# Kernel tuning notes

Hardware: AMD Instinct MI355X
Metric: run time of the kernel (lower is better)

The kernel has to match this reference:

```python
import jax, jax.numpy as jnp
import numpy as np

# Hard-coded dims from the module: 76 subcarriers * 12 data OFDM symbols = 912 data REs,
# QPSK (2 bits/sym), rate 1/2 -> n=1824, k=912; 4 tx streams, 8 rx antennas.
B, S, K = 512, 4, 912      # batch, streams, info bits (= data REs per stream)
R = 8                       # rx antennas
D = K                       # data resource elements per stream
N_CODE = 2 * K              # coded bits
SH1, SH2 = 7, 150           # circulant shifts of the LDPC-like code
BP_ITERS = 10
INV_SQRT2 = 0.7071067811865476

# check c connects info vars {c, c-7, c-150 (mod K)} and parity var K+c -> check degree 4
_c = np.arange(K)
VAR_IDX = jnp.asarray(np.stack([_c % K, (_c - SH1) % K, (_c - SH2) % K, K + _c], axis=1), jnp.int32)  # [K,4]


def setup_inputs() -> dict:
    key = jax.random.key(0)
    k1, k2, k3, k4, k5 = jax.random.split(key, 5)
    return {
        "b_bits": jax.random.randint(k1, (B, S, K), 0, 2, dtype=jnp.int32),
        "h_real": jax.random.normal(k2, (B, D, R, S), dtype=jnp.float32),
        "h_imag": jax.random.normal(k3, (B, D, R, S), dtype=jnp.float32),
        "n_real": jax.random.normal(k4, (B, D, R), dtype=jnp.float32),
        "n_imag": jax.random.normal(k5, (B, D, R), dtype=jnp.float32),
        "ebno_db": 10,
    }


def _bp_decode(llr):
    """Min-sum BP decode. llr: [B,S,N_CODE] demapper LLRs (log p1/p0). Returns hard info bits."""
    L = (-llr).reshape(B * S, N_CODE)          # internal convention log(p0/p1)
    vflat = VAR_IDX.reshape(-1)
    c2v = jnp.zeros((B * S, K, 4), L.dtype)
    pos = jnp.arange(4)
    for _ in range(BP_ITERS):
        ext = jnp.zeros_like(L).at[:, vflat].add(c2v.reshape(B * S, -1))
        tot = L + ext
        m_vc = tot[:, VAR_IDX] - c2v           # [BS,K,4] var->check
        a = jnp.abs(m_vc)
        srt = jnp.sort(a, -1)
        min1, min2 = srt[..., 0:1], srt[..., 1:2]
        amin = jnp.argmin(a, -1, keepdims=True)
        excl = jnp.where(pos == amin, min2, min1)   # leave-one-out min
        s = jnp.where(m_vc < 0, -1.0, 1.0)
        s_excl = jnp.prod(s, -1, keepdims=True) * s  # sign product excluding self
        c2v = s_excl * excl
    ext = jnp.zeros_like(L).at[:, vflat].add(c2v.reshape(B * S, -1))
    tot = L + ext
    return (tot[:, :K] < 0).astype(jnp.int32).reshape(B, S, K)


def reference(b_bits, h_real, h_imag, n_real, n_imag, ebno_db):
    no = 10.0 ** (-float(ebno_db) / 10.0)  # ebnodb2no with 2 bits/sym * rate 1/2
    # --- LDPC-like systematic circulant encode: p = A b mod 2, c = [b | p] ---
    p = (b_bits + jnp.roll(b_bits, SH1, -1) + jnp.roll(b_bits, SH2, -1)) % 2
    c = jnp.concatenate([b_bits, p], -1)                    # [B,S,N_CODE]
    # --- Gray QPSK mapper ---
    cb = c.reshape(B, S, K, 2).astype(jnp.float32)
    x = ((1.0 - 2.0 * cb[..., 0]) + 1j * (1.0 - 2.0 * cb[..., 1])) * INV_SQRT2  # [B,S,D]
    x_rg = jnp.transpose(x, (0, 2, 1))                      # [B,D,S]
    # --- normalized Rayleigh MIMO channel per RE + AWGN ---
    h = ((h_real + 1j * h_imag) * INV_SQRT2).astype(jnp.complex64)  # [B,D,R,S], E|h|^2=1
    noise = (n_real + 1j * n_imag).astype(jnp.complex64) * np.float32(np.sqrt(no * 0.5))
    y = jnp.einsum('bdrs,bds->bdr', h, x_rg) + noise        # [B,D,R]
    # --- per-RE LMMSE equalizer with Sionna-style bias normalization ---
    hH = jnp.conj(jnp.swapaxes(h, -1, -2))                  # [B,D,S,R]
    A = jnp.einsum('bdsr,bdrt->bdst', hH, h) + jnp.asarray(no, h.dtype) * jnp.eye(S, dtype=h.dtype)
    G = jnp.linalg.solve(A, hH)                             # [B,D,S,R]
    z = jnp.einsum('bdsr,bdr->bds', G, y)
    dgg = jnp.clip(jnp.real(jnp.einsum('bdsr,bdrs->bds', G, h)), 1e-6, 1.0 - 1e-6)
    x_hat = z / dgg.astype(jnp.complex64)
    no_eff = (1.0 - dgg) / dgg                              # [B,D,S]
    # --- exact APP QPSK demapper: llr = log p1/p0 ---
    scale = -2.0 * np.float32(np.sqrt(2.0)) / no_eff
    llr = jnp.stack([scale * jnp.real(x_hat), scale * jnp.imag(x_hat)], -1)  # [B,D,S,2]
    llr = jnp.transpose(llr, (0, 2, 1, 3)).reshape(B, S, N_CODE)
    # --- BP decode ---
    b_hat = _bp_decode(llr)
    return b_bits, b_hat
```

## Files before the change

### kernel.cpp

```cpp
#include <hip/hip_runtime.h>

#define B_ 512
#define S_ 4
#define K_ 912
#define R_ 8
#define D_ 912
#define NCODE 1824
#define BSK (B_*S_*K_)
#define BP_ITERS 10
#define NTH 228
#define CODES_OFF 16

__global__ void setup_kernel(const int* __restrict__ ebno, float* __restrict__ cst) {
  int ei = ebno[0];
  float ef = (ei >= -100 && ei <= 100) ? (float)ei : __int_as_float(ei);
  double no_d = pow(10.0, -(double)ef / 10.0);
  cst[0] = (float)no_d;
  cst[1] = (float)sqrt(no_d * 0.5);
}

__global__ __launch_bounds__(256) void pack_codes_kernel(
    const int* __restrict__ bbits, unsigned char* __restrict__ codes) {
  int g = blockIdx.x * 256 + threadIdx.x;
  int b = g / D_;
  int d = g - b * D_;
  int k2 = 2 * d;
  unsigned code = 0;
#pragma unroll
  for (int s = 0; s < S_; ++s) {
    const int* bb = bbits + (b * S_ + s) * K_;
    unsigned c0, c1;
    if (k2 < K_) {
      c0 = (unsigned)bb[k2];
      c1 = (unsigned)bb[k2 + 1];
    } else {
      int j0 = k2 - K_, j1 = k2 + 1 - K_;
      int j0a = j0 - 7;   if (j0a < 0) j0a += K_;
      int j0b = j0 - 150; if (j0b < 0) j0b += K_;
      c0 = (unsigned)(bb[j0] + bb[j0a] + bb[j0b]) & 1u;
      int j1a = j1 - 7;   if (j1a < 0) j1a += K_;
      int j1b = j1 - 150; if (j1b < 0) j1b += K_;
      c1 = (unsigned)(bb[j1] + bb[j1a] + bb[j1b]) & 1u;
    }
    code |= (c0 << (2 * s)) | (c1 << (2 * s + 1));
  }
  codes[g] = (unsigned char)code;
}

#define BFLY1(v) { v += __shfl_xor(v, 1); }

__global__ __launch_bounds__(256) void mmse_llr_kernel(
    const float* __restrict__ hre, const float* __restrict__ him,
    const float* __restrict__ nre, const float* __restrict__ nim,
    const float* __restrict__ cst, const unsigned char* __restrict__ codes,
    float* __restrict__ outf) {
#pragma clang fp contract(off)
  __shared__ float4 sre[1024];
  __shared__ float4 sim[1024];
  int tid = threadIdx.x;
  int t = blockIdx.x * 256 + tid;
  int g = t >> 1;
  int half = t & 1;
  int b = g / D_;
  int d = g - b * D_;
  int k2 = 2 * d;

  const float no_f = cst[0];
  const float nscale = cst[1];
  const float INV2 = 0.70710678118654752440f;

  const float4* hre4 = reinterpret_cast<const float4*>(hre);
  const float4* him4 = reinterpret_cast<const float4*>(him);
  size_t base = (size_t)blockIdx.x * 1024;
#pragma unroll
  for (int j = 0; j < 4; ++j) {
    int m = j * 256 + tid;
    int slot = (m & ~3) | ((m & 3) ^ ((m >> 3) & 3));
    sre[slot] = hre4[base + m];
    sim[slot] = him4[base + m];
  }

  float4 nr4v = reinterpret_cast<const float4*>(nre)[t];
  float4 ni4v = reinterpret_cast<const float4*>(nim)[t];
  unsigned code = codes[g];
  __syncthreads();

  float xr[S_], xq[S_];
#pragma unroll
  for (int s = 0; s < S_; ++s) {
    unsigned c0 = (code >> (2 * s)) & 1u;
    unsigned c1 = (code >> (2 * s + 1)) & 1u;
    xr[s] = __uint_as_float(0x3F3504F3u ^ (c0 << 31));
    xq[s] = __uint_as_float(0x3F3504F3u ^ (c1 << 31));
  }

  int gl = tid >> 1;
  int vb = gl * 8 + half * 4;
  int key = gl & 3;
  float4 hRq[4], hIq[4];
#pragma unroll
  for (int q = 0; q < 4; ++q) {
    int slot = vb + (q ^ key);
    hRq[q ^ key ? 0 : 0] = hRq[0];
  }
#pragma unroll
  for (int q = 0; q < 4; ++q) {
    hRq[q] = sre[vb + (q ^ key)];
    hIq[q] = sim[vb + (q ^ key)];
  }

  float nrv[4] = {nr4v.x, nr4v.y, nr4v.z, nr4v.w};
  float niv[4] = {ni4v.x, ni4v.y, ni4v.z, ni4v.w};

  float Ad0=0.f, Ad1=0.f, Ad2=0.f, Ad3=0.f;
  float A10r=0.f,A10i=0.f,A20r=0.f,A20i=0.f,A21r=0.f,A21i=0.f;
  float A30r=0.f,A30i=0.f,A31r=0.f,A31i=0.f,A32r=0.f,A32i=0.f;
  float w0r=0.f,w0i=0.f,w1r=0.f,w1i=0.f,w2r=0.f,w2i=0.f,w3r=0.f,w3i=0.f;

#pragma unroll
  for (int q = 0; q < 4; ++q) {
    float4 h4r = hRq[q];
    float4 h4i = hIq[q];
    float hr0=h4r.x*INV2, hr1=h4r.y*INV2, hr2=h4r.z*INV2, hr3=h4r.w*INV2;
    float hi0=h4i.x*INV2, hi1=h4i.y*INV2, hi2=h4i.z*INV2, hi3=h4i.w*INV2;
    float yr = 0.f, yi = 0.f;
    yr += hr0*xr[0] - hi0*xq[0]; yi += hr0*xq[0] + hi0*xr[0];
    yr += hr1*xr[1] - hi1*xq[1]; yi += hr1*xq[1] + hi1*xr[1];
    yr += hr2*xr[2] - hi2*xq[2]; yi += hr2*xq[2] + hi2*xr[2];
    yr += hr3*xr[3] - hi3*xq[3]; yi += hr3*xq[3] + hi3*xr[3];
    yr += nrv[q]*nscale; yi += niv[q]*nscale;
    Ad0 += hr0*hr0 + hi0*hi0;
    Ad1 += hr1*hr1 + hi1*hi1;
    Ad2 += hr2*hr2 + hi2*hi2;
    Ad3 += hr3*hr3 + hi3*hi3;
    A10r += hr1*hr0 + hi1*hi0;  A10i += hr1*hi0 - hi1*hr0;
    A20r += hr2*hr0 + hi2*hi0;  A20i += hr2*hi0 - hi2*hr0;
    A21r += hr2*hr1 + hi2*hi1;  A21i += hr2*hi1 - hi2*hr1;
    A30r += hr3*hr0 + hi3*hi0;  A30i += hr3*hi0 - hi3*hr0;
    A31r += hr3*hr1 + hi3*hi1;  A31i += hr3*hi1 - hi3*hr1;
    A32r += hr3*hr2 + hi3*hi2;  A32i += hr3*hi2 - hi3*hr2;
    w0r += hr0*yr + hi0*yi;  w0i += hr0*yi - hi0*yr;
    w1r += hr1*yr + hi1*yi;  w1i += hr1*yi - hi1*yr;
    w2r += hr2*yr + hi2*yi;  w2i += hr2*yi - hi2*yr;
    w3r += hr3*yr + hi3*yi;  w3i += hr3*yi - hi3*yr;
  }

  BFLY1(Ad0) BFLY1(Ad1) BFLY1(Ad2) BFLY1(Ad3)
  BFLY1(A10r) BFLY1(A10i) BFLY1(A20r) BFLY1(A20i) BFLY1(A21r) BFLY1(A21i)
  BFLY1(A30r) BFLY1(A30i) BFLY1(A31r) BFLY1(A31i) BFLY1(A32r) BFLY1(A32i)
  BFLY1(w0r) BFLY1(w0i) BFLY1(w1r) BFLY1(w1i)
  BFLY1(w2r) BFLY1(w2i) BFLY1(w3r) BFLY1(w3i)

  float Dv0 = Ad0 + no_f;
  float iD0 = 1.0f / Dv0;
  float L10r = A10r*iD0, L10i = A10i*iD0;
  float L20r = A20r*iD0, L20i = A20i*iD0;
  float L30r = A30r*iD0, L30i = A30i*iD0;
  float Dv1 = Ad1 + no_f - (L10r*L10r + L10i*L10i)*Dv0;
  float iD1 = 1.0f / Dv1;
  float t21r = A21r - (L20r*L10r + L20i*L10i)*Dv0;
  float t21i = A21i - (L20i*L10r - L20r*L10i)*Dv0;
  float L21r = t21r*iD1, L21i = t21i*iD1;
  float t31r = A31r - (L30r*L10r + L30i*L10i)*Dv0;
  float t31i = A31i - (L30i*L10r - L30r*L10i)*Dv0;
  float L31r = t31r*iD1, L31i = t31i*iD1;
  float Dv2 = Ad2 + no_f - (L20r*L20r + L20i*L20i)*Dv0 - (L21r*L21r + L21i*L21i)*Dv1;
  float iD2 = 1.0f / Dv2;
  float t32r = A32r - (L30r*L20r + L30i*L20i)*Dv0 - (L31r*L21r + L31i*L21i)*Dv1;
  float t32i = A32i - (L30i*L20r - L30r*L20i)*Dv0 - (L31i*L21r - L31r*L21i)*Dv1;
  float L32r = t32r*iD2, L32i = t32i*iD2;
  float Dv3 = Ad3 + no_f - (L30r*L30r + L30i*L30i)*Dv0 - (L31r*L31r + L31i*L31i)*Dv1
                        - (L32r*L32r + L32i*L32i)*Dv2;
  float iD3 = 1.0f / Dv3;

  float c0r = w0r, c0i = w0i;
  float c1r = w1r - (L10r*c0r - L10i*c0i);
  float c1i = w1i - (L10r*c0i + L10i*c0r);
  float c2r = w2r - (L20r*c0r - L20i*c0i) - (L21r*c1r - L21i*c1i);
  float c2i = w2i - (L20r*c0i + L20i*c0r) - (L21r*c1i + L21i*c1r);
  float c3r = w3r - (L30r*c0r - L30i*c0i) - (L31r*c1r - L31i*c1i) - (L32r*c2r - L32i*c2i);
  float c3i = w3i - (L30r*c0i + L30i*c0r) - (L31r*c1i + L31i*c1r) - (L32r*c2i + L32i*c2r);
  c0r *= iD0; c0i *= iD0;
  c1r *= iD1; c1i *= iD1;
  c2r *= iD2; c2i *= iD2;
  c3r *= iD3; c3i *= iD3;
  float z3r = c3r, z3i = c3i;
  float z2r = c2r - (L32r*z3r + L32i*z3i);
  float z2i = c2i - (L32r*z3i - L32i*z3r);
  float z1r = c1r - (L21r*z2r + L21i*z2i) - (L31r*z3r + L31i*z3i);
  float z1i = c1i - (L21r*z2i - L21i*z2r) - (L31r*z3i - L31i*z3r);
  float z0r = c0r - (L10r*z1r + L10i*z1i) - (L20r*z2r + L20i*z2i) - (L30r*z3r + L30i*z3i);
  float z0i = c0i - (L10r*z1i - L10i*z1r) - (L20r*z2i - L20i*z2r) - (L30r*z3i - L30i*z3r);

  float M10r = -L10r, M10i = -L10i;
  float M21r = -L21r, M21i = -L21i;
  float M32r = -L32r, M32i = -L32i;
  float M20r = -L20r - (L21r*M10r - L21i*M10i);
  float M20i = -L20i - (L21r*M10i + L21i*M10r);
  float M31r = -L31r - (L32r*M21r - L32i*M21i);
  float M31i = -L31i - (L32r*M21i + L32i*M21r);
  float M30r = -L30r - (L31r*M10r - L31i*M10i) - (L32r*M20r - L32i*M20i);
  float M30i = -L30i - (L31r*M10i + L31i*M10r) - (L32r*M20i + L32i*M20r);
  float Ai0 = iD0 + (M10r*M10r + M10i*M10i)*iD1 + (M20r*M20r + M20i*M20i)*iD2
                  + (M30r*M30r + M30i*M30i)*iD3;
  float Ai1 = iD1 + (M21r*M21r + M21i*M21i)*iD2 + (M31r*M31r + M31i*M31i)*iD3;
  float Ai2 = iD2 + (M32r*M32r + M32i*M32i)*iD3;
  float Ai3 = iD3;

  float zrv[4] = {z0r, z1r, z2r, z3r};
  float ziv[4] = {z0i, z1i, z2i, z3i};
  float Aiv[4] = {Ai0, Ai1, Ai2, Ai3};

#pragma unroll
  for (int j = 0; j < 2; ++j) {
    int s = half * 2 + j;
    float dgg = 1.0f - no_f * Aiv[s];
    float dg = fminf(fmaxf(dgg, 1e-6f), (float)(1.0 - 1e-6));
    float xhr = zrv[s] / dg;
    float xhi = ziv[s] / dg;
    float noe = (1.0f - dg) / dg;
    float sc = -2.8284270763397217f / noe;
    float2 o;
    o.x = -(sc * xhr);
    o.y = -(sc * xhi);
    size_t w = (size_t)(b * S_ + s);
    if (k2 < K_) {
      *reinterpret_cast<float2*>(outf + w * K_ + k2) = o;
    } else {
      *reinterpret_cast<float2*>(outf + (size_t)BSK + w * K_ + (k2 - K_)) = o;
    }
  }
}

__global__ __launch_bounds__(256) void bp_kernel(const int* __restrict__ bbits,
                                                 int* __restrict__ out) {
#pragma clang fp contract(off)
  __shared__ float tot[K_];
  __shared__ float E0[K_];
  __shared__ float E1[K_];
  __shared__ float E2[K_];
  int w = blockIdx.x;
  int tid = threadIdx.x;
  const float* outf = (const float*)out;
  bool act = tid < NTH;

  float Lv[4], LP[4];
  float c0v[4] = {0.f,0.f,0.f,0.f};
  float c1v[4] = {0.f,0.f,0.f,0.f};
  float c2v_[4] = {0.f,0.f,0.f,0.f};
  float c3v[4] = {0.f,0.f,0.f,0.f};

  if (act) {
#pragma unroll
    for (int k = 0; k < 4; ++k) {
      int n = tid + NTH * k;
      Lv[k] = outf[(size_t)w * K_ + n];
      LP[k] = outf[(size_t)BSK + (size_t)w * K_ + n];
      E0[n] = 0.f; E1[n] = 0.f; E2[n] = 0.f;
    }
  }
  __syncthreads();

  for (int it = 0; it < BP_ITERS; ++it) {
    if (act) {
#pragma unroll
      for (int k = 0; k < 4; ++k) {
        int n = tid + NTH * k;
        tot[n] = Lv[k] + ((E0[n] + E1[n]) + E2[n]);
      }
    }
    __syncthreads();
    if (act) {
#pragma unroll
      for (int k = 0; k < 4; ++k) {
        int c = tid + NTH * k;
        int i1 = c - 7;   if (i1 < 0) i1 += K_;
        int i2 = c - 150; if (i2 < 0) i2 += K_;
        float m0 = tot[c]  - c0v[k];
        float m1 = tot[i1] - c1v[k];
        float m2 = tot[i2] - c2v_[k];
        float totP = LP[k] + c3v[k];
        float m3 = totP - c3v[k];
        float a0 = fabsf(m0), a1 = fabsf(m1), a2 = fabsf(m2), a3 = fabsf(m3);
        float t01 = fminf(a0, a1), t23 = fminf(a2, a3);
        float e0 = fminf(a1, t23);
        float e1 = fminf(a0, t23);
        float e2 = fminf(t01, a3);
        float e3 = fminf(t01, a2);
        unsigned s0 = __float_as_uint(m0) & 0x80000000u;
        unsigned s1 = __float_as_uint(m1) & 0x80000000u;
        unsigned s2 = __float_as_uint(m2) & 0x80000000u;
        unsigned s3 = __float_as_uint(m3) & 0x80000000u;
        unsigned sp = (s0 ^ s1) ^ (s2 ^ s3);
        float n0 = __uint_as_float(__float_as_uint(e0) ^ (sp ^ s0));
        float n1 = __uint_as_float(__float_as_uint(e1) ^ (sp ^ s1));
        float n2 = __uint_as_float(__float_as_uint(e2) ^ (sp ^ s2));
        float n3 = __uint_as_float(__float_as_uint(e3) ^ (sp ^ s3));
        c0v[k] = n0; c1v[k] = n1; c2v_[k] = n2; c3v[k] = n3;
        E0[c] = n0; E1[i1] = n1; E2[i2] = n2;
      }
    }
    __syncthreads();
  }

  if (act) {
#pragma unroll
    for (int k = 0; k < 4; ++k) {
      int n = tid + NTH * k;
      float ttt = Lv[k] + ((E0[n] + E1[n]) + E2[n]);
      out[(size_t)BSK + (size_t)w * K_ + n] = (ttt < 0.f) ? 1 : 0;
      out[(size_t)w * K_ + n] = bbits[(size_t)w * K_ + n];
    }
  }
}

extern "C" void kernel_launch(void* const* d_in, const int* in_sizes, int n_in,
                              void* d_out, int out_size, void* d_ws, size_t ws_size,
                              hipStream_t stream) {
  const int*   b_bits = (const int*)d_in[0];
  const float* h_real = (const float*)d_in[1];
  const float* h_imag = (const float*)d_in[2];
  const float* n_real = (const float*)d_in[3];
  const float* n_imag = (const float*)d_in[4];
  const int*   ebno   = (const int*)d_in[5];
  int* out = (int*)d_out;
  float* cst = (float*)d_ws;
  unsigned char* codes = (unsigned char*)d_ws + CODES_OFF;

  setup_kernel<<<1, 1, 0, stream>>>(ebno, cst);
  pack_codes_kernel<<<(B_ * D_) / 256, 256, 0, stream>>>(b_bits, codes);
  mmse_llr_kernel<<<(B_ * D_ * 2) / 256, 256, 0, stream>>>(
      h_real, h_imag, n_real, n_imag, cst, codes, (float*)d_out);
  bp_kernel<<<B_ * S_, 256, 0, stream>>>(b_bits, out);
}
```

Before: 65.55 us.

## Restructure MMSE kernel: one thread per RE, two REs per thread, staged loads

The MMSE/LLR kernel changes from two threads per resource element (with shuffle reductions) to one thread handling two whole resource elements. Each 128-thread block covers 256 REs and streams the channel through shared memory in four phases of two rx antennas each. This removes the cross-lane butterflies and duplicated Cholesky solve, raising work per thread. In exchange, the 24-float accumulators for two REs raise register pressure, the grid has fewer threads, and each phase adds a barrier.

Measured after the change: 98.76 us. 50.7% more time.

```diff
diff --git a/kernel.cpp b/kernel.cpp
--- a/kernel.cpp
+++ b/kernel.cpp
@@ -3,13 +3,13 @@
 #define B_ 512
 #define S_ 4
 #define K_ 912
-#define R_ 8
 #define D_ 912
-#define NCODE 1824
 #define BSK (B_*S_*K_)
 #define BP_ITERS 10
 #define NTH 228
 #define CODES_OFF 16
+#define THB 128
+#define GRPB 256
 
 __global__ void setup_kernel(const int* __restrict__ ebno, float* __restrict__ cst) {
   int ei = ebno[0];
@@ -47,173 +47,112 @@
   codes[g] = (unsigned char)code;
 }
 
-#define BFLY1(v) { v += __shfl_xor(v, 1); }
-
-__global__ __launch_bounds__(256) void mmse_llr_kernel(
-    const float* __restrict__ hre, const float* __restrict__ him,
-    const float* __restrict__ nre, const float* __restrict__ nim,
-    const float* __restrict__ cst, const unsigned char* __restrict__ codes,
-    float* __restrict__ outf) {
+struct AccT {
+  float Ad0, Ad1, Ad2, Ad3;
+  float A10r, A10i, A20r, A20i, A21r, A21i;
+  float A30r, A30i, A31r, A31i, A32r, A32i;
+  float w0r, w0i, w1r, w1i, w2r, w2i, w3r, w3i;
+};
+
+__device__ __forceinline__ void accum(AccT& A, float4 h4r, float4 h4i,
+                                      const float* xr, const float* xq,
+                                      float nr, float ni, float nscale) {
 #pragma clang fp contract(off)
-  __shared__ float4 sre[1024];
-  __shared__ float4 sim[1024];
-  int tid = threadIdx.x;
-  int t = blockIdx.x * 256 + tid;
-  int g = t >> 1;
-  int half = t & 1;
-  int b = g / D_;
-  int d = g - b * D_;
-  int k2 = 2 * d;
-
-  const float no_f = cst[0];
-  const float nscale = cst[1];
   const float INV2 = 0.70710678118654752440f;
-
-  const float4* hre4 = reinterpret_cast<const float4*>(hre);
-  const float4* him4 = reinterpret_cast<const float4*>(him);
-  size_t base = (size_t)blockIdx.x * 1024;
-#pragma unroll
-  for (int j = 0; j < 4; ++j) {
-    int m = j * 256 + tid;
-    int slot = (m & ~3) | ((m & 3) ^ ((m >> 3) & 3));
-    sre[slot] = hre4[base + m];
-    sim[slot] = him4[base + m];
-  }
-
-  float4 nr4v = reinterpret_cast<const float4*>(nre)[t];
-  float4 ni4v = reinterpret_cast<const float4*>(nim)[t];
-  unsigned code = codes[g];
-  __syncthreads();
-
-  float xr[S_], xq[S_];
-#pragma unroll
-  for (int s = 0; s < S_; ++s) {
-    unsigned c0 = (code >> (2 * s)) & 1u;
-    unsigned c1 = (code >> (2 * s + 1)) & 1u;
-    xr[s] = __uint_as_float(0x3F3504F3u ^ (c0 << 31));
-    xq[s] = __uint_as_float(0x3F3504F3u ^ (c1 << 31));
-  }
-
-  int gl = tid >> 1;
-  int vb = gl * 8 + half * 4;
-  int key = gl & 3;
-  float4 hRq[4], hIq[4];
-#pragma unroll
-  for (int q = 0; q < 4; ++q) {
-    int slot = vb + (q ^ key);
-    hRq[q ^ key ? 0 : 0] = hRq[0];
-  }
-#pragma unroll
-  for (int q = 0; q < 4; ++q) {
-    hRq[q] = sre[vb + (q ^ key)];
-    hIq[q] = sim[vb + (q ^ key)];
-  }
-
-  float nrv[4] = {nr4v.x, nr4v.y, nr4v.z, nr4v.w};
-  float niv[4] = {ni4v.x, ni4v.y, ni4v.z, ni4v.w};
-
-  float Ad0=0.f, Ad1=0.f, Ad2=0.f, Ad3=0.f;
-  float A10r=0.f,A10i=0.f,A20r=0.f,A20i=0.f,A21r=0.f,A21i=0.f;
-  float A30r=0.f,A30i=0.f,A31r=0.f,A31i=0.f,A32r=0.f,A32i=0.f;
-  float w0r=0.f,w0i=0.f,w1r=0.f,w1i=0.f,w2r=0.f,w2i=0.f,w3r=0.f,w3i=0.f;
-
-#pragma unroll
-  for (int q = 0; q < 4; ++q) {
-    float4 h4r = hRq[q];
-    float4 h4i = hIq[q];
-    float hr0=h4r.x*INV2, hr1=h4r.y*INV2, hr2=h4r.z*INV2, hr3=h4r.w*INV2;
-    float hi0=h4i.x*INV2, hi1=h4i.y*INV2, hi2=h4i.z*INV2, hi3=h4i.w*INV2;
-    float yr = 0.f, yi = 0.f;
-    yr += hr0*xr[0] - hi0*xq[0]; yi += hr0*xq[0] + hi0*xr[0];
-    yr += hr1*xr[1] - hi1*xq[1]; yi += hr1*xq[1] + hi1*xr[1];
-    yr += hr2*xr[2] - hi2*xq[2]; yi += hr2*xq[2] + hi2*xr[2];
-    yr += hr3*xr[3] - hi3*xq[3]; yi += hr3*xq[3] + hi3*xr[3];
-    yr += nrv[q]*nscale; yi += niv[q]*nscale;
-    Ad0 += hr0*hr0 + hi0*hi0;
-    Ad1 += hr1*hr1 + hi1*hi1;
-    Ad2 += hr2*hr2 + hi2*hi2;
-    Ad3 += hr3*hr3 + hi3*hi3;
-    A10r += hr1*hr0 + hi1*hi0;  A10i += hr1*hi0 - hi1*hr0;
-    A20r += hr2*hr0 + hi2*hi0;  A20i += hr2*hi0 - hi2*hr0;
-    A21r += hr2*hr1 + hi2*hi1;  A21i += hr2*hi1 - hi2*hr1;
-    A30r += hr3*hr0 + hi3*hi0;  A30i += hr3*hi0 - hi3*hr0;
-    A31r += hr3*hr1 + hi3*hi1;  A31i += hr3*hi1 - hi3*hr1;
-    A32r += hr3*hr2 + hi3*hi2;  A32i += hr3*hi2 - hi3*hr2;
-    w0r += hr0*yr + hi0*yi;  w0i += hr0*yi - hi0*yr;
-    w1r += hr1*yr + hi1*yi;  w1i += hr1*yi - hi1*yr;
-    w2r += hr2*yr + hi2*yi;  w2i += hr2*yi - hi2*yr;
-    w3r += hr3*yr + hi3*yi;  w3i += hr3*yi - hi3*yr;
-  }
-
-  BFLY1(Ad0) BFLY1(Ad1) BFLY1(Ad2) BFLY1(Ad3)
-  BFLY1(A10r) BFLY1(A10i) BFLY1(A20r) BFLY1(A20i) BFLY1(A21r) BFLY1(A21i)
-  BFLY1(A30r) BFLY1(A30i) BFLY1(A31r) BFLY1(A31i) BFLY1(A32r) BFLY1(A32i)
-  BFLY1(w0r) BFLY1(w0i) BFLY1(w1r) BFLY1(w1i)
-  BFLY1(w2r) BFLY1(w2i) BFLY1(w3r) BFLY1(w3i)
-
-  float Dv0 = Ad0 + no_f;
+  float hr0 = h4r.x * INV2, hr1 = h4r.y * INV2, hr2 = h4r.z * INV2, hr3 = h4r.w * INV2;
+  float hi0 = h4i.x * INV2, hi1 = h4i.y * INV2, hi2 = h4i.z * INV2, hi3 = h4i.w * INV2;
+  float yr = 0.f, yi = 0.f;
+  yr += hr0 * xr[0] - hi0 * xq[0]; yi += hr0 * xq[0] + hi0 * xr[0];
+  yr += hr1 * xr[1] - hi1 * xq[1]; yi += hr1 * xq[1] + hi1 * xr[1];
+  yr += hr2 * xr[2] - hi2 * xq[2]; yi += hr2 * xq[2] + hi2 * xr[2];
+  yr += hr3 * xr[3] - hi3 * xq[3]; yi += hr3 * xq[3] + hi3 * xr[3];
+  yr += nr * nscale; yi += ni * nscale;
+  A.Ad0 += hr0 * hr0 + hi0 * hi0;
+  A.Ad1 += hr1 * hr1 + hi1 * hi1;
+  A.Ad2 += hr2 * hr2 + hi2 * hi2;
+  A.Ad3 += hr3 * hr3 + hi3 * hi3;
+  A.A10r += hr1 * hr0 + hi1 * hi0;  A.A10i += hr1 * hi0 - hi1 * hr0;
+  A.A20r += hr2 * hr0 + hi2 * hi0;  A.A20i += hr2 * hi0 - hi2 * hr0;
+  A.A21r += hr2 * hr1 + hi2 * hi1;  A.A21i += hr2 * hi1 - hi2 * hr1;
+  A.A30r += hr3 * hr0 + hi3 * hi0;  A.A30i += hr3 * hi0 - hi3 * hr0;
+  A.A31r += hr3 * hr1 + hi3 * hi1;  A.A31i += hr3 * hi1 - hi3 * hr1;
+  A.A32r += hr3 * hr2 + hi3 * hi2;  A.A32i += hr3 * hi2 - hi3 * hr2;
+  A.w0r += hr0 * yr + hi0 * yi;  A.w0i += hr0 * yi - hi0 * yr;
+  A.w1r += hr1 * yr + hi1 * yi;  A.w1i += hr1 * yi - hi1 * yr;
+  A.w2r += hr2 * yr + hi2 * yi;  A.w2i += hr2 * yi - hi2 * yr;
+  A.w3r += hr3 * yr + hi3 * yi;  A.w3i += hr3 * yi - hi3 * yr;
+}
+
+__device__ __forceinline__ void solve_write(const AccT& a, float no_f, int g,
+                                            float* __restrict__ outf) {
+#pragma clang fp contract(off)
+  float Dv0 = a.Ad0 + no_f;
   float iD0 = 1.0f / Dv0;
-  float L10r = A10r*iD0, L10i = A10i*iD0;
-  float L20r = A20r*iD0, L20i = A20i*iD0;
-  float L30r = A30r*iD0, L30i = A30i*iD0;
-  float Dv1 = Ad1 + no_f - (L10r*L10r + L10i*L10i)*Dv0;
+  float L10r = a.A10r * iD0, L10i = a.A10i * iD0;
+  float L20r = a.A20r * iD0, L20i = a.A20i * iD0;
+  float L30r = a.A30r * iD0, L30i = a.A30i * iD0;
+  float Dv1 = a.Ad1 + no_f - (L10r * L10r + L10i * L10i) * Dv0;
   float iD1 = 1.0f / Dv1;
-  float t21r = A21r - (L20r*L10r + L20i*L10i)*Dv0;
-  float t21i = A21i - (L20i*L10r - L20r*L10i)*Dv0;
-  float L21r = t21r*iD1, L21i = t21i*iD1;
-  float t31r = A31r - (L30r*L10r + L30i*L10i)*Dv0;
-  float t31i = A31i - (L30i*L10r - L30r*L10i)*Dv0;
-  float L31r = t31r*iD1, L31i = t31i*iD1;
-  float Dv2 = Ad2 + no_f - (L20r*L20r + L20i*L20i)*Dv0 - (L21r*L21r + L21i*L21i)*Dv1;
+  float t21r = a.A21r - (L20r * L10r + L20i * L10i) * Dv0;
+  float t21i = a.A21i - (L20i * L10r - L20r * L10i) * Dv0;
+  float L21r = t21r * iD1, L21i = t21i * iD1;
+  float t31r = a.A31r - (L30r * L10r + L30i * L10i) * Dv0;
+  float t31i = a.A31i - (L30i * L10r - L30r * L10i) * Dv0;
+  float L31r = t31r * iD1, L31i = t31i * iD1;
+  float Dv2 = a.Ad2 + no_f - (L20r * L20r + L20i * L20i) * Dv0
+                          - (L21r * L21r + L21i * L21i) * Dv1;
   float iD2 = 1.0f / Dv2;
-  float t32r = A32r - (L30r*L20r + L30i*L20i)*Dv0 - (L31r*L21r + L31i*L21i)*Dv1;
-  float t32i = A32i - (L30i*L20r - L30r*L20i)*Dv0 - (L31i*L21r - L31r*L21i)*Dv1;
-  float L32r = t32r*iD2, L32i = t32i*iD2;
-  float Dv3 = Ad3 + no_f - (L30r*L30r + L30i*L30i)*Dv0 - (L31r*L31r + L31i*L31i)*Dv1
-                        - (L32r*L32r + L32i*L32i)*Dv2;
+  float t32r = a.A32r - (L30r * L20r + L30i * L20i) * Dv0 - (L31r * L21r + L31i * L21i) * Dv1;
+  float t32i = a.A32i - (L30i * L20r - L30r * L20i) * Dv0 - (L31i * L21r - L31r * L21i) * Dv1;
+  float L32r = t32r * iD2, L32i = t32i * iD2;
+  float Dv3 = a.Ad3 + no_f - (L30r * L30r + L30i * L30i) * Dv0
+                          - (L31r * L31r + L31i * L31i) * Dv1
+                          - (L32r * L32r + L32i * L32i) * Dv2;
   float iD3 = 1.0f / Dv3;
 
-  float c0r = w0r, c0i = w0i;
-  float c1r = w1r - (L10r*c0r - L10i*c0i);
-  float c1i = w1i - (L10r*c0i + L10i*c0r);
-  float c2r = w2r - (L20r*c0r - L20i*c0i) - (L21r*c1r - L21i*c1i);
-  float c2i = w2i - (L20r*c0i + L20i*c0r) - (L21r*c1i + L21i*c1r);
-  float c3r = w3r - (L30r*c0r - L30i*c0i) - (L31r*c1r - L31i*c1i) - (L32r*c2r - L32i*c2i);
-  float c3i = w3i - (L30r*c0i + L30i*c0r) - (L31r*c1i + L31i*c1r) - (L32r*c2i + L32i*c2r);
+  float c0r = a.w0r, c0i = a.w0i;
+  float c1r = a.w1r - (L10r * c0r - L10i * c0i);
+  float c1i = a.w1i - (L10r * c0i + L10i * c0r);
+  float c2r = a.w2r - (L20r * c0r - L20i * c0i) - (L21r * c1r - L21i * c1i);
+  float c2i = a.w2i - (L20r * c0i + L20i * c0r) - (L21r * c1i + L21i * c1r);
+  float c3r = a.w3r - (L30r * c0r - L30i * c0i) - (L31r * c1r - L31i * c1i) - (L32r * c2r - L32i * c2i);
+  float c3i = a.w3i - (L30r * c0i + L30i * c0r) - (L31r * c1i + L31i * c1r) - (L32r * c2i + L32i * c2r);
   c0r *= iD0; c0i *= iD0;
   c1r *= iD1; c1i *= iD1;
   c2r *= iD2; c2i *= iD2;
   c3r *= iD3; c3i *= iD3;
   float z3r = c3r, z3i = c3i;
-  float z2r = c2r - (L32r*z3r + L32i*z3i);
-  float z2i = c2i - (L32r*z3i - L32i*z3r);
-  float z1r = c1r - (L21r*z2r + L21i*z2i) - (L31r*z3r + L31i*z3i);
-  float z1i = c1i - (L21r*z2i - L21i*z2r) - (L31r*z3i - L31i*z3r);
-  float z0r = c0r - (L10r*z1r + L10i*z1i) - (L20r*z2r + L20i*z2i) - (L30r*z3r + L30i*z3i);
-  float z0i = c0i - (L10r*z1i - L10i*z1r) - (L20r*z2i - L20i*z2r) - (L30r*z3i - L30i*z3r);
+  float z2r = c2r - (L32r * z3r + L32i * z3i);
+  float z2i = c2i - (L32r * z3i - L32i * z3r);
+  float z1r = c1r - (L21r * z2r + L21i * z2i) - (L31r * z3r + L31i * z3i);
+  float z1i = c1i - (L21r * z2i - L21i * z2r) - (L31r * z3i - L31i * z3r);
+  float z0r = c0r - (L10r * z1r + L10i * z1i) - (L20r * z2r + L20i * z2i) - (L30r * z3r + L30i * z3i);
+  float z0i = c0i - (L10r * z1i - L10i * z1r) - (L20r * z2i - L20i * z2r) - (L30r * z3i - L30i * z3r);
 
   float M10r = -L10r, M10i = -L10i;
   float M21r = -L21r, M21i = -L21i;
   float M32r = -L32r, M32i = -L32i;
-  float M20r = -L20r - (L21r*M10r - L21i*M10i);
-  float M20i = -L20i - (L21r*M10i + L21i*M10r);
-  float M31r = -L31r - (L32r*M21r - L32i*M21i);
-  float M31i = -L31i - (L32r*M21i + L32i*M21r);
-  float M30r = -L30r - (L31r*M10r - L31i*M10i) - (L32r*M20r - L32i*M20i);
-  float M30i = -L30i - (L31r*M10i + L31i*M10r) - (L32r*M20i + L32i*M20r);
-  float Ai0 = iD0 + (M10r*M10r + M10i*M10i)*iD1 + (M20r*M20r + M20i*M20i)*iD2
-                  + (M30r*M30r + M30i*M30i)*iD3;
-  float Ai1 = iD1 + (M21r*M21r + M21i*M21i)*iD2 + (M31r*M31r + M31i*M31i)*iD3;
-  float Ai2 = iD2 + (M32r*M32r + M32i*M32i)*iD3;
+  float M20r = -L20r - (L21r * M10r - L21i * M10i);
+  float M20i = -L20i - (L21r * M10i + L21i * M10r);
+  float M31r = -L31r - (L32r * M21r - L32i * M21i);
+  float M31i = -L31i - (L32r * M21i + L32i * M21r);
+  float M30r = -L30r - (L31r * M10r - L31i * M10i) - (L32r * M20r - L32i * M20i);
+  float M30i = -L30i - (L31r * M10i + L31i * M10r) - (L32r * M20i + L32i * M20r);
+  float Ai0 = iD0 + (M10r * M10r + M10i * M10i) * iD1 + (M20r * M20r + M20i * M20i) * iD2
+                  + (M30r * M30r + M30i * M30i) * iD3;
+  float Ai1 = iD1 + (M21r * M21r + M21i * M21i) * iD2 + (M31r * M31r + M31i * M31i) * iD3;
+  float Ai2 = iD2 + (M32r * M32r + M32i * M32i) * iD3;
   float Ai3 = iD3;
 
   float zrv[4] = {z0r, z1r, z2r, z3r};
   float ziv[4] = {z0i, z1i, z2i, z3i};
   float Aiv[4] = {Ai0, Ai1, Ai2, Ai3};
 
-#pragma unroll
-  for (int j = 0; j < 2; ++j) {
-    int s = half * 2 + j;
+  int b = g / D_;
+  int d = g - b * D_;
+  int k2 = 2 * d;
+#pragma unroll
+  for (int s = 0; s < S_; ++s) {
     float dgg = 1.0f - no_f * Aiv[s];
     float dg = fminf(fmaxf(dgg, 1e-6f), (float)(1.0 - 1e-6));
     float xhr = zrv[s] / dg;
@@ -232,6 +171,80 @@
   }
 }
 
+__global__ __launch_bounds__(THB) void mmse_llr_kernel(
+    const float* __restrict__ hre, const float* __restrict__ him,
+    const float* __restrict__ nre, const float* __restrict__ nim,
+    const float* __restrict__ cst, const unsigned char* __restrict__ codes,
+    float* __restrict__ outf) {
+#pragma clang fp contract(off)
+  __shared__ float4 sre[2 * GRPB];
+  __shared__ float4 sim[2 * GRPB];
+  int tid = threadIdx.x;
+  int G0 = blockIdx.x * GRPB;
+  int gA = G0 + tid;
+  int gB = G0 + THB + tid;
+
+  const float no_f = cst[0];
+  const float nscale = cst[1];
+
+  unsigned cA = codes[gA], cB = codes[gB];
+  float xrA[4], xqA[4], xrB[4], xqB[4];
+#pragma unroll
+  for (int s = 0; s < S_; ++s) {
+    xrA[s] = __uint_as_float(0x3F3504F3u ^ (((cA >> (2 * s)) & 1u) << 31));
+    xqA[s] = __uint_as_float(0x3F3504F3u ^ (((cA >> (2 * s + 1)) & 1u) << 31));
+    xrB[s] = __uint_as_float(0x3F3504F3u ^ (((cB >> (2 * s)) & 1u) << 31));
+    xqB[s] = __uint_as_float(0x3F3504F3u ^ (((cB >> (2 * s + 1)) & 1u) << 31));
+  }
+
+  const float4* hre4 = reinterpret_cast<const float4*>(hre);
+  const float4* him4 = reinterpret_cast<const float4*>(him);
+  const float4* nr4 = reinterpret_cast<const float4*>(nre);
+  const float4* ni4 = reinterpret_cast<const float4*>(nim);
+
+  AccT aA = {}, aB = {};
+  float4 nA4 = {}, niA4 = {}, nB4 = {}, niB4 = {};
+  int keyA = tid & 1;
+
+#pragma unroll
+  for (int h = 0; h < 4; ++h) {
+    if (h) __syncthreads();
+    if ((h & 1) == 0) {
+      int idx = h >> 1;
+      nA4  = nr4[(size_t)gA * 2 + idx];
+      niA4 = ni4[(size_t)gA * 2 + idx];
+      nB4  = nr4[(size_t)gB * 2 + idx];
+      niB4 = ni4[(size_t)gB * 2 + idx];
+    }
+#pragma unroll
+    for (int j = 0; j < 4; ++j) {
+      int m = j * THB + tid;
+      int gl = m >> 1, q = m & 1;
+      size_t gidx = (size_t)(G0 + gl) * 8 + h * 2 + q;
+      int slot = gl * 2 + (q ^ (gl & 1));
+      sre[slot] = hre4[gidx];
+      sim[slot] = him4[gidx];
+    }
+    __syncthreads();
+    float nrA0 = (h & 1) ? nA4.z  : nA4.x,  nrA1 = (h & 1) ? nA4.w  : nA4.y;
+    float niA0 = (h & 1) ? niA4.z : niA4.x, niA1 = (h & 1) ? niA4.w : niA4.y;
+    float nrB0 = (h & 1) ? nB4.z  : nB4.x,  nrB1 = (h & 1) ? nB4.w  : nB4.y;
+    float niB0 = (h & 1) ? niB4.z : niB4.x, niB1 = (h & 1) ? niB4.w : niB4.y;
+#pragma unroll
+    for (int q = 0; q < 2; ++q) {
+      float4 hr = sre[tid * 2 + (q ^ keyA)];
+      float4 hi = sim[tid * 2 + (q ^ keyA)];
+      accum(aA, hr, hi, xrA, xqA, q ? nrA1 : nrA0, q ? niA1 : niA0, nscale);
+      float4 hr2 = sre[(tid + THB) * 2 + (q ^ keyA)];
+      float4 hi2 = sim[(tid + THB) * 2 + (q ^ keyA)];
+      accum(aB, hr2, hi2, xrB, xqB, q ? nrB1 : nrB0, q ? niB1 : niB0, nscale);
+    }
+  }
+
+  solve_write(aA, no_f, gA, outf);
+  solve_write(aB, no_f, gB, outf);
+}
+
 __global__ __launch_bounds__(256) void bp_kernel(const int* __restrict__ bbits,
                                                  int* __restrict__ out) {
 #pragma clang fp contract(off)
@@ -245,10 +258,10 @@
   bool act = tid < NTH;
 
   float Lv[4], LP[4];
-  float c0v[4] = {0.f,0.f,0.f,0.f};
-  float c1v[4] = {0.f,0.f,0.f,0.f};
-  float c2v_[4] = {0.f,0.f,0.f,0.f};
-  float c3v[4] = {0.f,0.f,0.f,0.f};
+  float c0v[4] = {0.f, 0.f, 0.f, 0.f};
+  float c1v[4] = {0.f, 0.f, 0.f, 0.f};
+  float c2v_[4] = {0.f, 0.f, 0.f, 0.f};
+  float c3v[4] = {0.f, 0.f, 0.f, 0.f};
 
   if (act) {
 #pragma unroll
@@ -329,7 +342,7 @@
 
   setup_kernel<<<1, 1, 0, stream>>>(ebno, cst);
   pack_codes_kernel<<<(B_ * D_) / 256, 256, 0, stream>>>(b_bits, codes);
-  mmse_llr_kernel<<<(B_ * D_ * 2) / 256, 256, 0, stream>>>(
+  mmse_llr_kernel<<<(B_ * D_) / GRPB, THB, 0, stream>>>(
       h_real, h_imag, n_real, n_imag, cst, codes, (float*)d_out);
   bp_kernel<<<B_ * S_, 256, 0, stream>>>(b_bits, out);
 }
```

## Persistent grid-stride MMSE kernel with register prefetch and shared-memory code packing

Applied to the files above, without the earlier changes.

The MMSE/LLR kernel now runs a fixed grid of 912 blocks, and each thread handles four groups in a grid-stride loop. The next group's channel, noise and code data are prefetched into registers while the current group is computed, and the shared-memory transpose staging is replaced by direct per-thread float4 loads. pack_codes now runs one block per batch entry, stages that entry's bits in shared memory as bytes and computes parity with XOR, which cuts redundant global gathers. The trade-off is higher register pressure from the prefetch and uncoalesced strided per-thread float4 loads (64 B per thread) in place of the earlier coalesced shared-memory staging.

Measured after the change: 73.14 us. 11.6% more time.

```diff
diff --git a/kernel.cpp b/kernel.cpp
--- a/kernel.cpp
+++ b/kernel.cpp
@@ -5,11 +5,13 @@
 #define K_ 912
 #define R_ 8
 #define D_ 912
-#define NCODE 1824
+#define NG (B_*D_)
+#define NT (NG*2)
 #define BSK (B_*S_*K_)
 #define BP_ITERS 10
 #define NTH 228
 #define CODES_OFF 16
+#define MMSE_BLOCKS 912
 
 __global__ void setup_kernel(const int* __restrict__ ebno, float* __restrict__ cst) {
   int ei = ebno[0];
@@ -21,96 +23,67 @@
 
 __global__ __launch_bounds__(256) void pack_codes_kernel(
     const int* __restrict__ bbits, unsigned char* __restrict__ codes) {
-  int g = blockIdx.x * 256 + threadIdx.x;
-  int b = g / D_;
-  int d = g - b * D_;
-  int k2 = 2 * d;
-  unsigned code = 0;
-#pragma unroll
-  for (int s = 0; s < S_; ++s) {
-    const int* bb = bbits + (b * S_ + s) * K_;
-    unsigned c0, c1;
-    if (k2 < K_) {
-      c0 = (unsigned)bb[k2];
-      c1 = (unsigned)bb[k2 + 1];
-    } else {
-      int j0 = k2 - K_, j1 = k2 + 1 - K_;
-      int j0a = j0 - 7;   if (j0a < 0) j0a += K_;
-      int j0b = j0 - 150; if (j0b < 0) j0b += K_;
-      c0 = (unsigned)(bb[j0] + bb[j0a] + bb[j0b]) & 1u;
-      int j1a = j1 - 7;   if (j1a < 0) j1a += K_;
-      int j1b = j1 - 150; if (j1b < 0) j1b += K_;
-      c1 = (unsigned)(bb[j1] + bb[j1a] + bb[j1b]) & 1u;
-    }
-    code |= (c0 << (2 * s)) | (c1 << (2 * s + 1));
-  }
-  codes[g] = (unsigned char)code;
+  __shared__ unsigned char sb[S_ * K_];
+  int b = blockIdx.x;
+  int tid = threadIdx.x;
+  const int* row = bbits + (size_t)b * S_ * K_;
+  for (int i = tid; i < S_ * K_; i += 256) sb[i] = (unsigned char)row[i];
+  __syncthreads();
+#pragma unroll
+  for (int k = 0; k < 4; ++k) {
+    int d = tid + 256 * k;
+    if (d < D_) {
+      int k2 = 2 * d;
+      unsigned code = 0;
+#pragma unroll
+      for (int s = 0; s < S_; ++s) {
+        const unsigned char* bs = sb + s * K_;
+        unsigned c0, c1;
+        if (k2 < K_) {
+          c0 = bs[k2];
+          c1 = bs[k2 + 1];
+        } else {
+          int j0 = k2 - K_, j1 = k2 + 1 - K_;
+          int j0a = j0 - 7;   if (j0a < 0) j0a += K_;
+          int j0b = j0 - 150; if (j0b < 0) j0b += K_;
+          c0 = (unsigned)(bs[j0] ^ bs[j0a] ^ bs[j0b]);
+          int j1a = j1 - 7;   if (j1a < 0) j1a += K_;
+          int j1b = j1 - 150; if (j1b < 0) j1b += K_;
+          c1 = (unsigned)(bs[j1] ^ bs[j1a] ^ bs[j1b]);
+        }
+        code |= (c0 << (2 * s)) | (c1 << (2 * s + 1));
+      }
+      codes[b * D_ + d] = (unsigned char)code;
+    }
+  }
 }
 
 #define BFLY1(v) { v += __shfl_xor(v, 1); }
 
-__global__ __launch_bounds__(256) void mmse_llr_kernel(
-    const float* __restrict__ hre, const float* __restrict__ him,
-    const float* __restrict__ nre, const float* __restrict__ nim,
-    const float* __restrict__ cst, const unsigned char* __restrict__ codes,
-    float* __restrict__ outf) {
+__device__ __forceinline__ void compute_group(
+    float4 hR0, float4 hR1, float4 hR2, float4 hR3,
+    float4 hI0, float4 hI1, float4 hI2, float4 hI3,
+    float4 nr4v, float4 ni4v, unsigned code, int t,
+    float no_f, float nscale, float* __restrict__ outf) {
 #pragma clang fp contract(off)
-  __shared__ float4 sre[1024];
-  __shared__ float4 sim[1024];
-  int tid = threadIdx.x;
-  int t = blockIdx.x * 256 + tid;
   int g = t >> 1;
   int half = t & 1;
   int b = g / D_;
   int d = g - b * D_;
   int k2 = 2 * d;
-
-  const float no_f = cst[0];
-  const float nscale = cst[1];
   const float INV2 = 0.70710678118654752440f;
 
-  const float4* hre4 = reinterpret_cast<const float4*>(hre);
-  const float4* him4 = reinterpret_cast<const float4*>(him);
-  size_t base = (size_t)blockIdx.x * 1024;
-#pragma unroll
-  for (int j = 0; j < 4; ++j) {
-    int m = j * 256 + tid;
-    int slot = (m & ~3) | ((m & 3) ^ ((m >> 3) & 3));
-    sre[slot] = hre4[base + m];
-    sim[slot] = him4[base + m];
-  }
-
-  float4 nr4v = reinterpret_cast<const float4*>(nre)[t];
-  float4 ni4v = reinterpret_cast<const float4*>(nim)[t];
-  unsigned code = codes[g];
-  __syncthreads();
-
   float xr[S_], xq[S_];
 #pragma unroll
   for (int s = 0; s < S_; ++s) {
-    unsigned c0 = (code >> (2 * s)) & 1u;
-    unsigned c1 = (code >> (2 * s + 1)) & 1u;
-    xr[s] = __uint_as_float(0x3F3504F3u ^ (c0 << 31));
-    xq[s] = __uint_as_float(0x3F3504F3u ^ (c1 << 31));
-  }
-
-  int gl = tid >> 1;
-  int vb = gl * 8 + half * 4;
-  int key = gl & 3;
-  float4 hRq[4], hIq[4];
-#pragma unroll
-  for (int q = 0; q < 4; ++q) {
-    int slot = vb + (q ^ key);
-    hRq[q ^ key ? 0 : 0] = hRq[0];
-  }
-#pragma unroll
-  for (int q = 0; q < 4; ++q) {
-    hRq[q] = sre[vb + (q ^ key)];
-    hIq[q] = sim[vb + (q ^ key)];
+    xr[s] = __uint_as_float(0x3F3504F3u ^ (((code >> (2 * s)) & 1u) << 31));
+    xq[s] = __uint_as_float(0x3F3504F3u ^ (((code >> (2 * s + 1)) & 1u) << 31));
   }
 
   float nrv[4] = {nr4v.x, nr4v.y, nr4v.z, nr4v.w};
   float niv[4] = {ni4v.x, ni4v.y, ni4v.z, ni4v.w};
+  float4 hRq[4] = {hR0, hR1, hR2, hR3};
+  float4 hIq[4] = {hI0, hI1, hI2, hI3};
 
   float Ad0=0.f, Ad1=0.f, Ad2=0.f, Ad3=0.f;
   float A10r=0.f,A10i=0.f,A20r=0.f,A20i=0.f,A21r=0.f,A21i=0.f;
@@ -228,6 +201,62 @@
       *reinterpret_cast<float2*>(outf + w * K_ + k2) = o;
     } else {
       *reinterpret_cast<float2*>(outf + (size_t)BSK + w * K_ + (k2 - K_)) = o;
+    }
+  }
+}
+
+__global__ __launch_bounds__(256) void mmse_llr_kernel(
+    const float* __restrict__ hre, const float* __restrict__ him,
+    const float* __restrict__ nre, const float* __restrict__ nim,
+    const float* __restrict__ cst, const unsigned char* __restrict__ codes,
+    float* __restrict__ outf) {
+#pragma clang fp contract(off)
+  const int stride = MMSE_BLOCKS * 256;
+  int t = blockIdx.x * 256 + threadIdx.x;
+  const float no_f = cst[0];
+  const float nscale = cst[1];
+  const float4* hre4 = reinterpret_cast<const float4*>(hre);
+  const float4* him4 = reinterpret_cast<const float4*>(him);
+  const float4* nre4 = reinterpret_cast<const float4*>(nre);
+  const float4* nim4 = reinterpret_cast<const float4*>(nim);
+
+  float4 cR0 = hre4[(size_t)t * 4 + 0];
+  float4 cR1 = hre4[(size_t)t * 4 + 1];
+  float4 cR2 = hre4[(size_t)t * 4 + 2];
+  float4 cR3 = hre4[(size_t)t * 4 + 3];
+  float4 cI0 = him4[(size_t)t * 4 + 0];
+  float4 cI1 = him4[(size_t)t * 4 + 1];
+  float4 cI2 = him4[(size_t)t * 4 + 2];
+  float4 cI3 = him4[(size_t)t * 4 + 3];
+  float4 cNr = nre4[t];
+  float4 cNi = nim4[t];
+  unsigned cCode = codes[t >> 1];
+
+#pragma unroll
+  for (int it = 0; it < 4; ++it) {
+    int tn = t + stride;
+    float4 nR0, nR1, nR2, nR3, nI0, nI1, nI2, nI3, nNr, nNi;
+    unsigned nCode = 0;
+    if (it < 3) {
+      nR0 = hre4[(size_t)tn * 4 + 0];
+      nR1 = hre4[(size_t)tn * 4 + 1];
+      nR2 = hre4[(size_t)tn * 4 + 2];
+      nR3 = hre4[(size_t)tn * 4 + 3];
+      nI0 = him4[(size_t)tn * 4 + 0];
+      nI1 = him4[(size_t)tn * 4 + 1];
+      nI2 = him4[(size_t)tn * 4 + 2];
+      nI3 = him4[(size_t)tn * 4 + 3];
+      nNr = nre4[tn];
+      nNi = nim4[tn];
+      nCode = codes[tn >> 1];
+    }
+    compute_group(cR0, cR1, cR2, cR3, cI0, cI1, cI2, cI3,
+                  cNr, cNi, cCode, t, no_f, nscale, outf);
+    if (it < 3) {
+      cR0 = nR0; cR1 = nR1; cR2 = nR2; cR3 = nR3;
+      cI0 = nI0; cI1 = nI1; cI2 = nI2; cI3 = nI3;
+      cNr = nNr; cNi = nNi; cCode = nCode;
+      t = tn;
     }
   }
 }
@@ -328,8 +357,8 @@
   unsigned char* codes = (unsigned char*)d_ws + CODES_OFF;
 
   setup_kernel<<<1, 1, 0, stream>>>(ebno, cst);
-  pack_codes_kernel<<<(B_ * D_) / 256, 256, 0, stream>>>(b_bits, codes);
-  mmse_llr_kernel<<<(B_ * D_ * 2) / 256, 256, 0, stream>>>(
+  pack_codes_kernel<<<B_, 256, 0, stream>>>(b_bits, codes);
+  mmse_llr_kernel<<<MMSE_BLOCKS, 256, 0, stream>>>(
       h_real, h_imag, n_real, n_imag, cst, codes, (float*)d_out);
   bp_kernel<<<B_ * S_, 256, 0, stream>>>(b_bits, out);
 }
```
